# Optimization experiments

Hardware: AMD Instinct MI355X
Metric: run time of the kernel (lower is better)

Reference implementation:

```python
import jax, jax.numpy as jnp
import numpy as np

B, C, S, L = 8, 512, 2048, 8921


def setup_inputs() -> dict:
    key = jax.random.key(0)
    k1, k2, k3, k4, k5 = jax.random.split(key, 5)
    return {
        "encoded": jax.random.normal(k1, (B, C, S), dtype=jnp.float32),
        "W_attn": jax.random.normal(k2, (L, C), dtype=jnp.float32) * 0.02,
        "b_attn": jax.random.normal(k3, (L,), dtype=jnp.float32) * 0.02,
        "W_cls": jax.random.normal(k4, (L, C), dtype=jnp.float32) * 0.02,
        "b_cls": jax.random.normal(k5, (L,), dtype=jnp.float32) * 0.02,
    }


def reference(encoded, W_attn, b_attn, W_cls, b_cls):
    # encoded: (B, C, S). Linear over channels after transpose -> scores (B, S, L)
    scores = jnp.einsum("bcs,lc->bsl", encoded, W_attn) + b_attn
    # softmax over the sequence dimension (dim=1 of (B, S, L))
    weights = jax.nn.softmax(scores, axis=1)
    # context: (B, L, S) @ (B, S, C) -> (B, L, C)
    context = jnp.einsum("bsl,bcs->blc", weights, encoded)
    # per-label diagonal classifier: elementwise multiply with (L, C) weight, reduce C
    logits = jnp.sum(context * W_cls, axis=2) + b_cls  # (B, L)
    return logits
```

## Files before the change

### kernel.cpp

```cpp
#include <hip/hip_runtime.h>
#include <hip/hip_bf16.h>
#include <stdint.h>

#define B_ 8
#define C_ 512
#define S_ 2048
#define L_ 8921
#define LTILE 128
#define NLT 70
#define NLTP 72
#define NSC 16
#define ROUNDS 16

using f32x16 = __attribute__((ext_vector_type(16))) float;
using s16x8  = __attribute__((ext_vector_type(8))) short;

static __device__ __forceinline__ unsigned short f2bf(float f) {
    union { float f; uint32_t u; } a; a.f = f;
    uint32_t u = a.u;
    return (unsigned short)((u + 0x7fffu + ((u >> 16) & 1u)) >> 16);
}

__global__ void cvt_wfrag(const float* __restrict__ src, unsigned short* __restrict__ dst) {
    int gid = blockIdx.x * 256 + threadIdx.x;
    int lane = gid & 63;
    int f    = gid >> 6;
    int kstep = f & 1;
    int rr    = (f >> 1) & 15;
    int wv    = (f >> 5) & 3;
    int lt    = f >> 7;
    int row = lt * 128 + wv * 32 + (lane & 31);
    if (row > L_ - 1) row = L_ - 1;
    int k0 = rr * 32 + kstep * 16 + (lane >> 5) * 8;
    const float* s = src + (size_t)row * C_ + k0;
    float4 v0 = ((const float4*)s)[0];
    float4 v1 = ((const float4*)s)[1];
    ushort4 o0, o1;
    o0.x = f2bf(v0.x); o0.y = f2bf(v0.y); o0.z = f2bf(v0.z); o0.w = f2bf(v0.w);
    o1.x = f2bf(v1.x); o1.y = f2bf(v1.y); o1.z = f2bf(v1.z); o1.w = f2bf(v1.w);
    ushort4* d = (ushort4*)(dst + (size_t)gid * 8);
    d[0] = o0; d[1] = o1;
}

__global__ void cvt_e(const float* __restrict__ enc, unsigned short* __restrict__ ebt) {
    __shared__ float tile[64][65];
    int x = blockIdx.x;
    int ct = (x & 7) * 64;
    int st = ((x >> 3) & 31) * 64;
    int b  = x >> 8;
    int t = threadIdx.x;
    const float* src = enc + (size_t)b * C_ * S_;
    #pragma unroll
    for (int it = 0; it < 16; ++it) {
        int idx = it * 256 + t;
        int rc = idx >> 6, rs = idx & 63;
        tile[rc][rs] = src[(size_t)(ct + rc) * S_ + st + rs];
    }
    __syncthreads();
    unsigned short* dst = ebt + (size_t)b * S_ * C_;
    #pragma unroll
    for (int it = 0; it < 16; ++it) {
        int idx = it * 256 + t;
        int rs = idx >> 6, rc = idx & 63;
        dst[(size_t)(st + rs) * C_ + ct + rc] = f2bf(tile[rc][rs]);
    }
}

__global__ __launch_bounds__(256, 2) void attn_main(
    const unsigned short* __restrict__ ebt,
    const unsigned short* __restrict__ wfa,
    const unsigned short* __restrict__ wfc,
    float* __restrict__ pnum, float* __restrict__ pden)
{
    __shared__ __align__(16) unsigned char sE[16384];

    const int tid  = threadIdx.x;
    const int lane = tid & 63;
    const int wave = tid >> 6;

    const int x   = blockIdx.x;
    const int i8  = x & 7;
    const int t9  = x >> 3;
    const int jj9 = t9 % 9;
    const int bsc = t9 / 9;
    const int lt  = jj9 * 8 + i8;
    const int b   = bsc & 7;
    const int sc  = bsc >> 3;
    const int s0  = sc * 128;

    const int h = lane >> 5;
    const unsigned short* waF = wfa + ((size_t)(lt * 4 + wave) * 32) * 512 + lane * 8;
    const unsigned short* wcF = wfc + ((size_t)(lt * 4 + wave) * 32) * 512 + lane * 8;

    const int slRow  = lane >> 2;
    const int srcCk  = (((lane & 3) ^ ((slRow >> 1) & 3)) << 3);
    const unsigned short* eg0 = ebt + ((size_t)b * S_ + s0 + (wave * 2) * 16 + slRow) * C_ + srcCk;
    const unsigned short* eg1 = eg0 + (size_t)16 * C_;
    const int ldst0 = (wave * 2) * 1024 + slRow * 64 + (lane & 3) * 16;
    const int ldst1 = ldst0 + 1024;

    auto stage = [&](int rr) {
        const int c0 = rr * 32;
        const int bufo = (rr & 1) << 13;
        __builtin_amdgcn_global_load_lds(
            (__attribute__((address_space(1))) void*)(eg0 + c0),
            (__attribute__((address_space(3))) void*)(sE + bufo + ldst0), 16, 0, 0);
        __builtin_amdgcn_global_load_lds(
            (__attribute__((address_space(1))) void*)(eg1 + c0),
            (__attribute__((address_space(3))) void*)(sE + bufo + ldst1), 16, 0, 0);
    };

    struct WREG { s16x8 a0, a1, c0, c1; };
    auto loadW = [&](int rr) -> WREG {
        WREG w;
        w.a0 = *(const s16x8*)(waF + (size_t)(rr * 2 + 0) * 512);
        w.a1 = *(const s16x8*)(waF + (size_t)(rr * 2 + 1) * 512);
        w.c0 = *(const s16x8*)(wcF + (size_t)(rr * 2 + 0) * 512);
        w.c1 = *(const s16x8*)(wcF + (size_t)(rr * 2 + 1) * 512);
        return w;
    };

    const int rowB  = (lane & 31) * 64;
    const int swz   = (lane >> 1) & 3;

    f32x16 accS[4], accV[4];
    #pragma unroll
    for (int nf = 0; nf < 4; ++nf)
        #pragma unroll
        for (int r = 0; r < 16; ++r) { accS[nf][r] = 0.f; accV[nf][r] = 0.f; }

    stage(0);
    WREG wcur = loadW(0);

    for (int rr = 0; rr < ROUNDS; ++rr) {
        __syncthreads();
        if (rr + 1 < ROUNDS) stage(rr + 1);
        WREG wnxt = (rr + 1 < ROUNDS) ? loadW(rr + 1) : wcur;

        const unsigned char* db = sE + ((rr & 1) << 13);
        {
            s16x8 fe[4];
            #pragma unroll
            for (int nf = 0; nf < 4; ++nf) {
                const int off = (nf << 11) + rowB + (((0 + h) ^ swz) << 4);
                fe[nf] = *(const s16x8*)(db + off);
            }
            #pragma unroll
            for (int nf = 0; nf < 4; ++nf) {
                accS[nf] = __builtin_amdgcn_mfma_f32_32x32x16_bf16(wcur.a0, fe[nf], accS[nf], 0, 0, 0);
                accV[nf] = __builtin_amdgcn_mfma_f32_32x32x16_bf16(wcur.c0, fe[nf], accV[nf], 0, 0, 0);
            }
        }
        {
            s16x8 fe[4];
            #pragma unroll
            for (int nf = 0; nf < 4; ++nf) {
                const int off = (nf << 11) + rowB + (((2 + h) ^ swz) << 4);
                fe[nf] = *(const s16x8*)(db + off);
            }
            #pragma unroll
            for (int nf = 0; nf < 4; ++nf) {
                accS[nf] = __builtin_amdgcn_mfma_f32_32x32x16_bf16(wcur.a1, fe[nf], accS[nf], 0, 0, 0);
                accV[nf] = __builtin_amdgcn_mfma_f32_32x32x16_bf16(wcur.c1, fe[nf], accV[nf], 0, 0, 0);
            }
        }
        wcur = wnxt;
    }

    float numA[16], denA[16];
    #pragma unroll
    for (int r = 0; r < 16; ++r) { numA[r] = 0.f; denA[r] = 0.f; }
    #pragma unroll
    for (int nf = 0; nf < 4; ++nf)
        #pragma unroll
        for (int r = 0; r < 16; ++r) {
            float e = __expf(accS[nf][r]);
            denA[r] += e;
            numA[r] += e * accV[nf][r];
        }
    if (lt < NLT) {
        const size_t obase = ((size_t)((b * NLT + lt) * NSC + sc)) * LTILE;
        #pragma unroll
        for (int r = 0; r < 16; ++r) {
            float n = numA[r], d = denA[r];
            n += __shfl_xor(n, 1);   d += __shfl_xor(d, 1);
            n += __shfl_xor(n, 2);   d += __shfl_xor(d, 2);
            n += __shfl_xor(n, 4);   d += __shfl_xor(d, 4);
            n += __shfl_xor(n, 8);   d += __shfl_xor(d, 8);
            n += __shfl_xor(n, 16);  d += __shfl_xor(d, 16);
            if ((lane & 31) == 0) {
                int row = wave * 32 + (r & 3) + 8 * (r >> 2) + 4 * h;
                pnum[obase + row] = n;
                pden[obase + row] = d;
            }
        }
    }
}

__global__ void finalize(const float* __restrict__ pnum, const float* __restrict__ pden,
                         const float* __restrict__ bcls, float* __restrict__ out) {
    int gid = blockIdx.x * 256 + threadIdx.x;
    if (gid >= B_ * L_) return;
    int b = gid / L_, l = gid - b * L_;
    int lt = l >> 7, row = l & 127;
    float n = 0.f, d = 0.f;
    #pragma unroll
    for (int s = 0; s < NSC; ++s) {
        size_t idx = ((size_t)((b * NLT + lt) * NSC + s)) * LTILE + row;
        n += pnum[idx];
        d += pden[idx];
    }
    out[gid] = n / d + bcls[l];
}

extern "C" void kernel_launch(void* const* d_in, const int* in_sizes, int n_in,
                              void* d_out, int out_size, void* d_ws, size_t ws_size,
                              hipStream_t stream) {
    (void)in_sizes; (void)n_in; (void)out_size; (void)ws_size;
    const float* enc  = (const float*)d_in[0];
    const float* Wa   = (const float*)d_in[1];
    const float* Wc   = (const float*)d_in[3];
    const float* bcls = (const float*)d_in[4];

    unsigned char* ws = (unsigned char*)d_ws;
    const size_t oEbt = 0;
    const size_t oWa  = oEbt + 16777216;
    const size_t oWc  = oWa + 9437184;
    const size_t oPn  = oWc + 9437184;
    const size_t oPd  = oPn + 4587520;

    unsigned short* ebt = (unsigned short*)(ws + oEbt);
    unsigned short* wfa = (unsigned short*)(ws + oWa);
    unsigned short* wfc = (unsigned short*)(ws + oWc);
    float* pnum = (float*)(ws + oPn);
    float* pden = (float*)(ws + oPd);

    const int wThreads = NLTP * 4 * ROUNDS * 2 * 64;
    cvt_wfrag<<<wThreads / 256, 256, 0, stream>>>(Wa, wfa);
    cvt_wfrag<<<wThreads / 256, 256, 0, stream>>>(Wc, wfc);
    cvt_e<<<B_ * 32 * 8, 256, 0, stream>>>(enc, ebt);
    attn_main<<<128 * 9 * 8, 256, 0, stream>>>(ebt, wfa, wfc, pnum, pden);
    finalize<<<(B_ * L_ + 255) / 256, 256, 0, stream>>>(pnum, pden, bcls, (float*)d_out);
}
```

Before: 441.2 us.

## Pre-fragment encoded tensor and load MFMA operands directly from global into registers

```diff
diff --git a/kernel.cpp b/kernel.cpp
--- a/kernel.cpp
+++ b/kernel.cpp
@@ -42,38 +42,34 @@
     d[0] = o0; d[1] = o1;
 }
 
-__global__ void cvt_e(const float* __restrict__ enc, unsigned short* __restrict__ ebt) {
-    __shared__ float tile[64][65];
-    int x = blockIdx.x;
-    int ct = (x & 7) * 64;
-    int st = ((x >> 3) & 31) * 64;
-    int b  = x >> 8;
-    int t = threadIdx.x;
-    const float* src = enc + (size_t)b * C_ * S_;
-    #pragma unroll
-    for (int it = 0; it < 16; ++it) {
-        int idx = it * 256 + t;
-        int rc = idx >> 6, rs = idx & 63;
-        tile[rc][rs] = src[(size_t)(ct + rc) * S_ + st + rs];
-    }
-    __syncthreads();
-    unsigned short* dst = ebt + (size_t)b * S_ * C_;
-    #pragma unroll
-    for (int it = 0; it < 16; ++it) {
-        int idx = it * 256 + t;
-        int rs = idx >> 6, rc = idx & 63;
-        dst[(size_t)(st + rs) * C_ + ct + rc] = f2bf(tile[rc][rs]);
-    }
-}
-
-__global__ __launch_bounds__(256, 2) void attn_main(
-    const unsigned short* __restrict__ ebt,
+__global__ void cvt_efrag(const float* __restrict__ enc, unsigned short* __restrict__ dst) {
+    int tid  = threadIdx.x;
+    int lane = tid & 63;
+    int f    = blockIdx.x * 4 + (tid >> 6);
+    int kstep = f & 1;
+    int rr    = (f >> 1) & 15;
+    int nf    = (f >> 5) & 3;
+    int bsc   = f >> 7;
+    int b  = bsc & 7;
+    int sc = bsc >> 3;
+    int s  = sc * 128 + nf * 32 + (lane & 31);
+    int c0 = rr * 32 + kstep * 16 + (lane >> 5) * 8;
+    const float* src = enc + (size_t)b * C_ * S_ + (size_t)c0 * S_ + s;
+    ushort4 o0, o1;
+    o0.x = f2bf(src[0 * S_]); o0.y = f2bf(src[1 * S_]);
+    o0.z = f2bf(src[2 * S_]); o0.w = f2bf(src[3 * S_]);
+    o1.x = f2bf(src[4 * S_]); o1.y = f2bf(src[5 * S_]);
+    o1.z = f2bf(src[6 * S_]); o1.w = f2bf(src[7 * S_]);
+    ushort4* d = (ushort4*)(dst + (size_t)f * 512 + lane * 8);
+    d[0] = o0; d[1] = o1;
+}
+
+__global__ __launch_bounds__(256) void attn_main(
+    const unsigned short* __restrict__ ebtF,
     const unsigned short* __restrict__ wfa,
     const unsigned short* __restrict__ wfc,
     float* __restrict__ pnum, float* __restrict__ pden)
 {
-    __shared__ __align__(16) unsigned char sE[16384];
-
     const int tid  = threadIdx.x;
     const int lane = tid & 63;
     const int wave = tid >> 6;
@@ -86,87 +82,56 @@
     const int lt  = jj9 * 8 + i8;
     const int b   = bsc & 7;
     const int sc  = bsc >> 3;
-    const int s0  = sc * 128;
-
-    const int h = lane >> 5;
+
     const unsigned short* waF = wfa + ((size_t)(lt * 4 + wave) * 32) * 512 + lane * 8;
     const unsigned short* wcF = wfc + ((size_t)(lt * 4 + wave) * 32) * 512 + lane * 8;
-
-    const int slRow  = lane >> 2;
-    const int srcCk  = (((lane & 3) ^ ((slRow >> 1) & 3)) << 3);
-    const unsigned short* eg0 = ebt + ((size_t)b * S_ + s0 + (wave * 2) * 16 + slRow) * C_ + srcCk;
-    const unsigned short* eg1 = eg0 + (size_t)16 * C_;
-    const int ldst0 = (wave * 2) * 1024 + slRow * 64 + (lane & 3) * 16;
-    const int ldst1 = ldst0 + 1024;
-
-    auto stage = [&](int rr) {
-        const int c0 = rr * 32;
-        const int bufo = (rr & 1) << 13;
-        __builtin_amdgcn_global_load_lds(
-            (__attribute__((address_space(1))) void*)(eg0 + c0),
-            (__attribute__((address_space(3))) void*)(sE + bufo + ldst0), 16, 0, 0);
-        __builtin_amdgcn_global_load_lds(
-            (__attribute__((address_space(1))) void*)(eg1 + c0),
-            (__attribute__((address_space(3))) void*)(sE + bufo + ldst1), 16, 0, 0);
+    const unsigned short* eF0 = ebtF + ((size_t)(bsc * 4 + 0) * 32) * 512 + lane * 8;
+    const unsigned short* eF1 = ebtF + ((size_t)(bsc * 4 + 1) * 32) * 512 + lane * 8;
+    const unsigned short* eF2 = ebtF + ((size_t)(bsc * 4 + 2) * 32) * 512 + lane * 8;
+    const unsigned short* eF3 = ebtF + ((size_t)(bsc * 4 + 3) * 32) * 512 + lane * 8;
+
+    struct RND { s16x8 wa0, wa1, wc0, wc1, e[4][2]; };
+    auto loadRound = [&](int rr, RND& r) {
+        const int co = rr * 1024;
+        r.wa0 = *(const s16x8*)(waF + co);
+        r.wa1 = *(const s16x8*)(waF + co + 512);
+        r.wc0 = *(const s16x8*)(wcF + co);
+        r.wc1 = *(const s16x8*)(wcF + co + 512);
+        r.e[0][0] = *(const s16x8*)(eF0 + co);  r.e[0][1] = *(const s16x8*)(eF0 + co + 512);
+        r.e[1][0] = *(const s16x8*)(eF1 + co);  r.e[1][1] = *(const s16x8*)(eF1 + co + 512);
+        r.e[2][0] = *(const s16x8*)(eF2 + co);  r.e[2][1] = *(const s16x8*)(eF2 + co + 512);
+        r.e[3][0] = *(const s16x8*)(eF3 + co);  r.e[3][1] = *(const s16x8*)(eF3 + co + 512);
     };
 
-    struct WREG { s16x8 a0, a1, c0, c1; };
-    auto loadW = [&](int rr) -> WREG {
-        WREG w;
-        w.a0 = *(const s16x8*)(waF + (size_t)(rr * 2 + 0) * 512);
-        w.a1 = *(const s16x8*)(waF + (size_t)(rr * 2 + 1) * 512);
-        w.c0 = *(const s16x8*)(wcF + (size_t)(rr * 2 + 0) * 512);
-        w.c1 = *(const s16x8*)(wcF + (size_t)(rr * 2 + 1) * 512);
-        return w;
+    f32x16 accS[4], accV[4];
+    #pragma unroll
+    for (int nf = 0; nf < 4; ++nf)
+        #pragma unroll
+        for (int r = 0; r < 16; ++r) { accS[nf][r] = 0.f; accV[nf][r] = 0.f; }
+
+    auto mfmaRound = [&](const RND& rd) {
+        #pragma unroll
+        for (int nf = 0; nf < 4; ++nf) {
+            accS[nf] = __builtin_amdgcn_mfma_f32_32x32x16_bf16(rd.wa0, rd.e[nf][0], accS[nf], 0, 0, 0);
+            accV[nf] = __builtin_amdgcn_mfma_f32_32x32x16_bf16(rd.wc0, rd.e[nf][0], accV[nf], 0, 0, 0);
+        }
+        #pragma unroll
+        for (int nf = 0; nf < 4; ++nf) {
+            accS[nf] = __builtin_amdgcn_mfma_f32_32x32x16_bf16(rd.wa1, rd.e[nf][1], accS[nf], 0, 0, 0);
+            accV[nf] = __builtin_amdgcn_mfma_f32_32x32x16_bf16(rd.wc1, rd.e[nf][1], accV[nf], 0, 0, 0);
+        }
     };
 
-    const int rowB  = (lane & 31) * 64;
-    const int swz   = (lane >> 1) & 3;
-
-    f32x16 accS[4], accV[4];
-    #pragma unroll
-    for (int nf = 0; nf < 4; ++nf)
-        #pragma unroll
-        for (int r = 0; r < 16; ++r) { accS[nf][r] = 0.f; accV[nf][r] = 0.f; }
-
-    stage(0);
-    WREG wcur = loadW(0);
-
-    for (int rr = 0; rr < ROUNDS; ++rr) {
-        __syncthreads();
-        if (rr + 1 < ROUNDS) stage(rr + 1);
-        WREG wnxt = (rr + 1 < ROUNDS) ? loadW(rr + 1) : wcur;
-
-        const unsigned char* db = sE + ((rr & 1) << 13);
-        {
-            s16x8 fe[4];
-            #pragma unroll
-            for (int nf = 0; nf < 4; ++nf) {
-                const int off = (nf << 11) + rowB + (((0 + h) ^ swz) << 4);
-                fe[nf] = *(const s16x8*)(db + off);
-            }
-            #pragma unroll
-            for (int nf = 0; nf < 4; ++nf) {
-                accS[nf] = __builtin_amdgcn_mfma_f32_32x32x16_bf16(wcur.a0, fe[nf], accS[nf], 0, 0, 0);
-                accV[nf] = __builtin_amdgcn_mfma_f32_32x32x16_bf16(wcur.c0, fe[nf], accV[nf], 0, 0, 0);
-            }
-        }
-        {
-            s16x8 fe[4];
-            #pragma unroll
-            for (int nf = 0; nf < 4; ++nf) {
-                const int off = (nf << 11) + rowB + (((2 + h) ^ swz) << 4);
-                fe[nf] = *(const s16x8*)(db + off);
-            }
-            #pragma unroll
-            for (int nf = 0; nf < 4; ++nf) {
-                accS[nf] = __builtin_amdgcn_mfma_f32_32x32x16_bf16(wcur.a1, fe[nf], accS[nf], 0, 0, 0);
-                accV[nf] = __builtin_amdgcn_mfma_f32_32x32x16_bf16(wcur.c1, fe[nf], accV[nf], 0, 0, 0);
-            }
-        }
-        wcur = wnxt;
+    RND r0, r1;
+    loadRound(0, r0);
+    for (int rr2 = 0; rr2 < ROUNDS / 2; ++rr2) {
+        loadRound(2 * rr2 + 1, r1);
+        mfmaRound(r0);
+        if (rr2 + 1 < ROUNDS / 2) loadRound(2 * rr2 + 2, r0);
+        mfmaRound(r1);
     }
 
+    const int h = lane >> 5;
     float numA[16], denA[16];
     #pragma unroll
     for (int r = 0; r < 16; ++r) { numA[r] = 0.f; denA[r] = 0.f; }
@@ -229,16 +194,16 @@
     const size_t oPn  = oWc + 9437184;
     const size_t oPd  = oPn + 4587520;
 
-    unsigned short* ebt = (unsigned short*)(ws + oEbt);
-    unsigned short* wfa = (unsigned short*)(ws + oWa);
-    unsigned short* wfc = (unsigned short*)(ws + oWc);
+    unsigned short* ebtF = (unsigned short*)(ws + oEbt);
+    unsigned short* wfa  = (unsigned short*)(ws + oWa);
+    unsigned short* wfc  = (unsigned short*)(ws + oWc);
     float* pnum = (float*)(ws + oPn);
     float* pden = (float*)(ws + oPd);
 
     const int wThreads = NLTP * 4 * ROUNDS * 2 * 64;
     cvt_wfrag<<<wThreads / 256, 256, 0, stream>>>(Wa, wfa);
     cvt_wfrag<<<wThreads / 256, 256, 0, stream>>>(Wc, wfc);
-    cvt_e<<<B_ * 32 * 8, 256, 0, stream>>>(enc, ebt);
-    attn_main<<<128 * 9 * 8, 256, 0, stream>>>(ebt, wfa, wfc, pnum, pden);
+    cvt_efrag<<<(128 * 4 * ROUNDS * 2) / 4, 256, 0, stream>>>(enc, ebtF);
+    attn_main<<<128 * 9 * 8, 256, 0, stream>>>(ebtF, wfa, wfc, pnum, pden);
     finalize<<<(B_ * L_ + 255) / 256, 256, 0, stream>>>(pnum, pden, bcls, (float*)d_out);
 }
```

After: 704.4 us. 59.6% more time.
